# Performance work log

Hardware: AMD Instinct MI355X
Metric: run time of the kernel (lower is better)

Reference implementation:

```python
import jax, jax.numpy as jnp
import numpy as np

N_NODES = 20000
N_EDGES = 400000
DIM = 128       # dim
NB = 16         # radial basis size
ZD = 16         # species encoding dim
N_SPECIES = 51
CUTOFF = 5.0
NLAYERS = 2
N_ONSITE = 3


def radial_basis(r):
    # 'gaussian_rinv': gaussians placed uniformly in inverse-distance space (HIP-NN style)
    rinv = 1.0 / r
    mus = jnp.linspace(1.0 / CUTOFF, 1.0, NB, dtype=r.dtype)
    sigma = mus[1] - mus[0]
    return jnp.exp(-0.5 * ((rinv[:, None] - mus[None, :]) / sigma) ** 2)  # [E, NB]


def setup_inputs() -> dict:
    key = jax.random.key(0)
    ks = jax.random.split(key, 16)
    species = jax.random.randint(ks[0], (N_NODES,), 1, N_SPECIES)
    edge_src = jax.random.randint(ks[1], (N_EDGES,), 0, N_NODES)
    edge_dst = jax.random.randint(ks[2], (N_EDGES,), 0, N_NODES)
    distances = jax.random.uniform(ks[3], (N_EDGES,), minval=0.8, maxval=CUTOFF)
    switch = jax.random.uniform(ks[4], (N_EDGES,))
    Z = jax.random.normal(ks[5], (N_SPECIES, ZD))  # species encoding table
    Ws0 = jax.random.normal(ks[6], (ZD, DIM)) / np.sqrt(ZD)
    bs0 = jnp.zeros((DIM,), jnp.float32)
    V0 = jax.random.normal(ks[7], (NB, ZD, DIM)) / np.sqrt(NB * ZD)
    Ws1 = jax.random.normal(ks[8], (DIM, DIM)) / np.sqrt(DIM)
    bs1 = jnp.zeros((DIM,), jnp.float32)
    V1 = jax.random.normal(ks[9], (NB, DIM, DIM)) / np.sqrt(NB * DIM)
    Won_a = jax.random.normal(ks[10], (NLAYERS, N_ONSITE, DIM, DIM)) / np.sqrt(DIM)
    bon_a = jnp.zeros((NLAYERS, N_ONSITE, DIM), jnp.float32)
    Won_b = jax.random.normal(ks[11], (NLAYERS, N_ONSITE, DIM, DIM)) / np.sqrt(DIM)
    bon_b = jnp.zeros((NLAYERS, N_ONSITE, DIM), jnp.float32)
    return dict(species=species, edge_src=edge_src, edge_dst=edge_dst,
                distances=distances, switch=switch, Z=Z,
                Ws0=Ws0, bs0=bs0, V0=V0, Ws1=Ws1, bs1=bs1, V1=V1,
                Won_a=Won_a, bon_a=bon_a, Won_b=Won_b, bon_b=bon_b)


def reference(species, edge_src, edge_dst, distances, switch, Z,
              Ws0, bs0, V0, Ws1, bs1, V1, Won_a, bon_a, Won_b, bon_b):
    zi = Z[species]                       # [N, ZD] species encoding
    s = radial_basis(distances)           # [E, NB] (identical basis each layer)
    sw = switch[:, None]                  # [E, 1]
    Ws, bs, Vs = (Ws0, Ws1), (bs0, bs1), (V0, V1)
    zis = []
    for layer in range(NLAYERS):
        zself = zi @ Ws[layer] + bs[layer]                        # [N, DIM]
        # mij = einsum('ej,ek,jkl->el', s, zi[edge_dst], V): per-edge outer then one GEMM
        zdst = zi[edge_dst]                                       # [E, k] gather
        outer = s[:, :, None] * zdst[:, None, :]                  # [E, NB, k]
        mij = outer.reshape(outer.shape[0], -1) @ Vs[layer].reshape(-1, DIM)  # [E, DIM]
        zi = jax.nn.silu(zself.at[edge_src].add(mij * sw))        # scatter-add
        for j in range(N_ONSITE):                                 # residual 2-layer MLPs
            h = jax.nn.silu(zi @ Won_a[layer, j] + bon_a[layer, j])
            zi = zi + h @ Won_b[layer, j] + bon_b[layer, j]
        zis.append(zi)
    # (embedding, embedding_layers)
    return zi, jnp.stack(zis, axis=1)
```

## Files before the change

### kernel.cpp

```cpp
#include <hip/hip_runtime.h>
#include <stdint.h>

#define NNODES 20000
#define NEDGES 400000
#define MTILES 1250
#define KS1 68

typedef __attribute__((ext_vector_type(8))) short short8;
typedef __attribute__((ext_vector_type(4))) float floatx4;

__device__ __forceinline__ float bf2f(uint16_t u){ return __uint_as_float(((uint32_t)u)<<16); }
__device__ __forceinline__ uint16_t f2bf(float f){
  uint32_t x = __float_as_uint(f);
  x += 0x7FFFu + ((x>>16)&1u);
  return (uint16_t)(x>>16);
}
__device__ __forceinline__ uint32_t packbf(float a, float b){
  return (uint32_t)f2bf(a) | ((uint32_t)f2bf(b)<<16);
}
__device__ __forceinline__ float siluf(float x){ return x/(1.0f+__expf(-x)); }
__device__ __forceinline__ float ldf(const void* p, int i, int md){
  return (md==1) ? bf2f(((const uint16_t*)p)[i]) : ((const float*)p)[i];
}

#define OFF_V0   0
#define N_V0     32768
#define OFF_WS1  32768
#define N_WS1    16384
#define OFF_BS1  49152
#define N_BS1    128
#define OFF_V1   49280
#define N_V1     262144
#define OFF_WA   311424
#define N_WA     98304
#define OFF_BA   409728
#define N_BA     768
#define OFF_WB   410496
#define N_WB     98304
#define OFF_BB   508800
#define N_BB     768
#define N_CONV   509568

__global__ void k_probe(const void* dist, int* mode){
  if(threadIdx.x != 0 || blockIdx.x != 0) return;
  const float* f = (const float*)dist;
  const uint16_t* h = (const uint16_t*)dist;
  int okf = 1, okb = 1;
  for(int i=0;i<256;i++){
    float a = f[i];       okf &= (a >= 0.7f) & (a <= 5.1f);
    float b = bf2f(h[i]); okb &= (b >= 0.7f) & (b <= 5.1f);
  }
  *mode = okb ? 1 : (okf ? 0 : 1);
}

__global__ __launch_bounds__(256) void k_conv(const void* s0,const void* s1,const void* s2,const void* s3,
                                              const void* s4,const void* s5,const void* s6,const void* s7,
                                              const int* __restrict__ modep, float* __restrict__ dst){
  int md = *modep;
  int i = blockIdx.x*256 + threadIdx.x;
  if(i >= N_CONV) return;
  const void* src; int t = i;
  if(t < N_V0){src=s0;}
  else if((t-=N_V0) < N_WS1){src=s1;}
  else if((t-=N_WS1) < N_BS1){src=s2;}
  else if((t-=N_BS1) < N_V1){src=s3;}
  else if((t-=N_V1) < N_WA){src=s4;}
  else if((t-=N_WA) < N_BA){src=s5;}
  else if((t-=N_BA) < N_WB){src=s6;}
  else {t-=N_WB; src=s7;}
  dst[i] = ldf(src, t, md);
}

__global__ __launch_bounds__(256) void k_hist(const int* __restrict__ src, int* __restrict__ cnt){
  int e = blockIdx.x*256 + threadIdx.x;
  if(e < NEDGES){
    int s = src[e];
    if((unsigned)s < NNODES) atomicAdd(&cnt[s], 1);
  }
}

__global__ __launch_bounds__(1024) void k_scan(int* cnt_cur, int* offs){
  __shared__ int wsum[16];
  int t = threadIdx.x;
  const int chunk = (NNODES + 1023)/1024;
  int lo = t*chunk, hi = lo+chunk;
  if(lo > NNODES) lo = NNODES;
  if(hi > NNODES) hi = NNODES;
  int s = 0;
  for(int i=lo;i<hi;i++) s += cnt_cur[i];
  int lane = t&63, wv = t>>6;
  int v = s;
  #pragma unroll
  for(int d=1; d<64; d<<=1){
    int u = __shfl_up(v, d);
    if(lane >= d) v += u;
  }
  if(lane==63) wsum[wv] = v;
  __syncthreads();
  if(t==0){
    int run = 0;
    #pragma unroll
    for(int i=0;i<16;i++){ int c = wsum[i]; wsum[i] = run; run += c; }
  }
  __syncthreads();
  int run = wsum[wv] + (v - s);
  for(int i=lo;i<hi;i++){
    int c = cnt_cur[i];
    offs[i] = run;
    cnt_cur[i] = run;
    run += c;
  }
  if(t==1023) offs[NNODES] = run;
}

__global__ __launch_bounds__(256) void k_fill(const int* __restrict__ src,
                                              const int* __restrict__ edst,
                                              const int* __restrict__ species,
                                              int* __restrict__ cur,
                                              int* __restrict__ dsts,
                                              int* __restrict__ sps,
                                              int* __restrict__ pos){
  int e = blockIdx.x*256 + threadIdx.x;
  if(e >= NEDGES) return;
  int s = src[e];
  if((unsigned)s >= NNODES) s = 0;
  int p = atomicAdd(&cur[s], 1);
  if((unsigned)p >= NEDGES) p = 0;
  pos[e] = p;
  int dn = edst[e];
  if((unsigned)dn >= NNODES) dn = 0;
  dsts[p] = dn;
  int sp = species[dn];
  if((unsigned)sp >= 51) sp = 0;
  sps[p] = sp;
}

__global__ __launch_bounds__(256) void k_G(const void* __restrict__ dist,
                                           const void* __restrict__ sw,
                                           const int* __restrict__ modep,
                                           const int* __restrict__ pos,
                                           uint16_t* __restrict__ gs){
  int e = blockIdx.x*256 + threadIdx.x;
  if(e >= NEDGES) return;
  int md = *modep;
  float r = ldf(dist, e, md);
  float w = ldf(sw, e, md);
  float rinv = 1.0f/r;
  const float sigma = 0.8f/15.0f;
  const float isig  = 15.0f/0.8f;
  uint32_t u[8];
  #pragma unroll
  for(int j=0;j<8;j++){
    float mu0 = 0.2f + sigma*(float)(2*j);
    float mu1 = 0.2f + sigma*(float)(2*j+1);
    float t0 = (rinv-mu0)*isig, t1 = (rinv-mu1)*isig;
    u[j] = packbf(w*__expf(-0.5f*t0*t0), w*__expf(-0.5f*t1*t1));
  }
  int p = pos[e];
  uint4* o = (uint4*)(gs + (size_t)p*16);
  o[0] = make_uint4(u[0],u[1],u[2],u[3]);
  o[1] = make_uint4(u[4],u[5],u[6],u[7]);
}

__global__ __launch_bounds__(128) void k_spec(const void* __restrict__ Z,
                                              const void* __restrict__ Ws0,
                                              const void* __restrict__ bs0,
                                              const int* __restrict__ modep,
                                              float* __restrict__ ZWs0,
                                              uint16_t* __restrict__ zfb){
  int s = blockIdx.x, d = threadIdx.x;
  int md = *modep;
  float zk[16];
  #pragma unroll
  for(int k=0;k<16;k++) zk[k] = ldf(Z, s*16+k, md);
  float a = ldf(bs0, d, md);
  #pragma unroll
  for(int k=0;k<16;k++) a = fmaf(zk[k], ldf(Ws0, k*128+d, md), a);
  ZWs0[s*128+d] = a;
  if(d < 16) zfb[s*16+d] = f2bf(zk[d]);
}

__global__ __launch_bounds__(256) void k_prepB(const float* __restrict__ W, int Ksteps,
                                               uint16_t* __restrict__ Bf){
  int idx = blockIdx.x*256 + threadIdx.x;
  int total = Ksteps*8*64;
  if(idx >= total) return;
  int l = idx & 63, nt = (idx>>6)&7, kk = idx>>9;
  int kbase = kk*32 + (l>>4)*8;
  int dim = nt*16 + (l&15);
  uint32_t u[4];
  #pragma unroll
  for(int t=0;t<4;t++){
    float f0 = W[(size_t)(kbase+2*t)*128 + dim];
    float f1 = W[(size_t)(kbase+2*t+1)*128 + dim];
    u[t] = packbf(f0,f1);
  }
  ((uint4*)Bf)[idx] = make_uint4(u[0],u[1],u[2],u[3]);
}

__global__ __launch_bounds__(256) void k_prepW(const float* __restrict__ conv,
                                               uint16_t* __restrict__ Wf){
  int idx = blockIdx.x*256 + threadIdx.x;
  if(idx >= 12*2048) return;
  int wi = idx>>11, r = idx&2047;
  int l = r & 63, nt = (r>>6)&7, kk = r>>9;
  const float* W = conv + ((wi<6) ? (OFF_WA + wi*16384) : (OFF_WB + (wi-6)*16384));
  int kbase = kk*32 + (l>>4)*8;
  int dim = nt*16 + (l&15);
  uint32_t u[4];
  #pragma unroll
  for(int t=0;t<4;t++){
    float f0 = W[(size_t)(kbase+2*t)*128 + dim];
    float f1 = W[(size_t)(kbase+2*t+1)*128 + dim];
    u[t] = packbf(f0,f1);
  }
  ((uint4*)Wf)[idx] = make_uint4(u[0],u[1],u[2],u[3]);
}

__global__ __launch_bounds__(256) void k_msg0f(const int* __restrict__ offs,
                                               const int* __restrict__ sps,
                                               const uint16_t* __restrict__ gs,
                                               const uint16_t* __restrict__ zfb,
                                               const uint16_t* __restrict__ Bf,
                                               const int* __restrict__ species,
                                               const float* __restrict__ ZWs0,
                                               float* __restrict__ zi){
  __shared__ uint16_t ldsA[8*64*8];
  int w = threadIdx.x>>6, l = threadIdx.x&63;
  int n0 = blockIdx.x*16;
  int col = l&15, quad = l>>4;
  for(int i=0;i<4;i++){
    int m = w*4 + i;
    int n = n0 + m;
    int beg = offs[n], end = offs[n+1];
    floatx4 acc0 = (floatx4){0.f,0.f,0.f,0.f};
    for(int p0=beg; p0<end; p0+=32){
      int sp[8];
      union { short8 s; uint16_t u[8]; } Bg, Az;
      #pragma unroll
      for(int j=0;j<8;j++){
        int p = p0 + quad*8 + j;
        int pc = p < end ? p : beg;
        sp[j] = sps[pc];
        uint16_t g = gs[(size_t)pc*16 + col];
        Bg.u[j] = (p < end) ? g : (uint16_t)0;
      }
      #pragma unroll
      for(int j=0;j<8;j++)
        Az.u[j] = zfb[sp[j]*16 + col];
      acc0 = __builtin_amdgcn_mfma_f32_16x16x32_bf16(Az.s, Bg.s, acc0, 0,0,0);
    }
    int K0 = col*16 + quad*4;
    int kk = K0>>5, qt = (K0>>3)&3, jt = K0&7;
    int slot = kk*64 + ((qt*16 + m) ^ (kk>>2));
    uint32_t lo = packbf(acc0[0], acc0[1]);
    uint32_t hi = packbf(acc0[2], acc0[3]);
    *(uint2*)(&ldsA[slot*8 + jt]) = make_uint2(lo, hi);
  }
  __syncthreads();
  floatx4 acc1 = (floatx4){0.f,0.f,0.f,0.f};
  floatx4 acc2 = (floatx4){0.f,0.f,0.f,0.f};
  const short8* Bp = (const short8*)Bf;
  int nt1 = w, nt2 = w+4;
  #pragma unroll
  for(int kk=0;kk<8;kk++){
    short8 a = *(const short8*)(&ldsA[(kk*64 + (l^(kk>>2)))*8]);
    short8 b1 = Bp[(size_t)(kk*8+nt1)*64 + l];
    short8 b2 = Bp[(size_t)(kk*8+nt2)*64 + l];
    acc1 = __builtin_amdgcn_mfma_f32_16x16x32_bf16(a, b1, acc1, 0,0,0);
    acc2 = __builtin_amdgcn_mfma_f32_16x16x32_bf16(a, b2, acc2, 0,0,0);
  }
  #pragma unroll
  for(int reg=0;reg<4;reg++){
    int node = n0 + quad*4 + reg;
    int sp = species[node];
    if((unsigned)sp >= 51) sp = 0;
    int d1 = nt1*16 + col, d2 = nt2*16 + col;
    zi[(size_t)node*128 + d1] = siluf(acc1[reg] + ZWs0[sp*128 + d1]);
    zi[(size_t)node*128 + d2] = siluf(acc2[reg] + ZWs0[sp*128 + d2]);
  }
}

__global__ __launch_bounds__(512) void k_msg1f(const int* __restrict__ offs,
                                               const int* __restrict__ dsts,
                                               const uint16_t* __restrict__ gs,
                                               const uint16_t* __restrict__ zib,
                                               const uint16_t* __restrict__ zib2,
                                               const uint16_t* __restrict__ Bf,
                                               const float* __restrict__ bias,
                                               float* __restrict__ zacc){
  __shared__ uint16_t ldsA[64*64*8];
  int w = threadIdx.x>>6, l = threadIdx.x&63;
  int n0 = blockIdx.x*16;
  int col = l&15, quad = l>>4;
  for(int i=0;i<2;i++){
    int m = w*2 + i;
    int n = n0 + m;
    int beg = offs[n], end = offs[n+1];
    floatx4 acc[8];
    #pragma unroll
    for(int t=0;t<8;t++) acc[t] = (floatx4){0.f,0.f,0.f,0.f};
    for(int p0=beg; p0<end; p0+=32){
      int dn[8];
      union { short8 s; uint16_t u[8]; } Bg;
      #pragma unroll
      for(int j=0;j<8;j++){
        int p = p0 + quad*8 + j;
        int pc = p < end ? p : beg;
        dn[j] = dsts[pc];
        uint16_t g = gs[(size_t)pc*16 + col];
        Bg.u[j] = (p < end) ? g : (uint16_t)0;
      }
      uint4 row[8];
      #pragma unroll
      for(int j=0;j<8;j++)
        row[j] = *(const uint4*)(zib2 + (size_t)dn[j]*128 + col*8);
      #pragma unroll
      for(int mt=0;mt<8;mt++){
        union { short8 s; uint32_t u32[4]; } Az;
        #pragma unroll
        for(int cp=0;cp<4;cp++){
          uint32_t a = ((const uint32_t*)&row[2*cp])[mt>>1];
          uint32_t b = ((const uint32_t*)&row[2*cp+1])[mt>>1];
          Az.u32[cp] = __builtin_amdgcn_perm(b, a, (mt&1) ? 0x07060302u : 0x05040100u);
        }
        acc[mt] = __builtin_amdgcn_mfma_f32_16x16x32_bf16(Az.s, Bg.s, acc[mt], 0,0,0);
      }
    }
    #pragma unroll
    for(int mt=0;mt<8;mt++){
      int K0 = col*128 + mt*16 + quad*4;
      int kk = K0>>5, qt = (K0>>3)&3, jt = K0&7;
      int slot = kk*64 + ((qt*16 + m) ^ (kk>>2));
      uint32_t lo = packbf(acc[mt][0], acc[mt][1]);
      uint32_t hi = packbf(acc[mt][2], acc[mt][3]);
      *(uint2*)(&ldsA[slot*8 + jt]) = make_uint2(lo, hi);
    }
  }
  __syncthreads();
  floatx4 acc1 = (floatx4){0.f,0.f,0.f,0.f};
  const short8* Bp = (const short8*)Bf;
  for(int kk=0;kk<64;kk++){
    short8 a = *(const short8*)(&ldsA[(kk*64 + (l^(kk>>2)))*8]);
    short8 b1 = Bp[(size_t)(kk*8+w)*64 + l];
    acc1 = __builtin_amdgcn_mfma_f32_16x16x32_bf16(a, b1, acc1, 0,0,0);
  }
  #pragma unroll
  for(int kk=64;kk<KS1;kk++){
    uint4 za = *(const uint4*)(zib + (size_t)(n0+col)*128 + (kk-64)*32 + quad*8);
    union { short8 s; uint4 u; } A; A.u = za;
    short8 b1 = Bp[(size_t)(kk*8+w)*64 + l];
    acc1 = __builtin_amdgcn_mfma_f32_16x16x32_bf16(A.s, b1, acc1, 0,0,0);
  }
  #pragma unroll
  for(int reg=0;reg<4;reg++){
    int node = n0 + quad*4 + reg;
    int d1 = w*16 + col;
    zacc[(size_t)node*128 + d1] = siluf(acc1[reg] + bias[d1]);
  }
}

__global__ __launch_bounds__(256) void k_onsite(float* __restrict__ zi,
                                                const uint16_t* __restrict__ Waf,
                                                const float* __restrict__ ba,
                                                const uint16_t* __restrict__ Wbf,
                                                const float* __restrict__ bb,
                                                void* __restrict__ outb,
                                                long off1, int st1,
                                                long off2, int st2,
                                                const int* __restrict__ modep,
                                                uint16_t* __restrict__ zib,
                                                uint16_t* __restrict__ zib2){
  __shared__ float zb[16*132];
  __shared__ float hb[16*132];
  int w = threadIdx.x>>6, l = threadIdx.x&63;
  int mtile = blockIdx.x;
  int n0 = mtile*16;
  int md = *modep;
  #pragma unroll
  for(int i=0;i<2;i++){
    int flat = (i*256 + threadIdx.x)*4;
    int node = flat>>7, k = flat&127;
    *(float4*)(zb + node*132 + k) = *(const float4*)(zi + (size_t)(n0+node)*128 + k);
  }
  __syncthreads();
  int m = l&15, q = l>>4;
  for(int j=0;j<3;j++){
    const short8* Ba = (const short8*)Waf + (size_t)j*2048 + l;
    floatx4 acc[2];
    acc[0] = (floatx4){0.f,0.f,0.f,0.f};
    acc[1] = (floatx4){0.f,0.f,0.f,0.f};
    #pragma unroll
    for(int kk=0;kk<4;kk++){
      const float* zp = zb + m*132 + kk*32 + q*8;
      float4 a0 = *(const float4*)zp, a1 = *(const float4*)(zp+4);
      union { short8 s; uint32_t u[4]; } A;
      A.u[0]=packbf(a0.x,a0.y); A.u[1]=packbf(a0.z,a0.w);
      A.u[2]=packbf(a1.x,a1.y); A.u[3]=packbf(a1.z,a1.w);
      #pragma unroll
      for(int t=0;t<2;t++){
        short8 bfr = Ba[(size_t)(kk*8 + w*2+t)*64];
        acc[t] = __builtin_amdgcn_mfma_f32_16x16x32_bf16(A.s, bfr, acc[t], 0,0,0);
      }
    }
    #pragma unroll
    for(int t=0;t<2;t++){
      int dim = (w*2+t)*16 + m;
      float bv = ba[j*128+dim];
      #pragma unroll
      for(int reg=0;reg<4;reg++)
        hb[(q*4+reg)*132 + dim] = siluf(acc[t][reg] + bv);
    }
    __syncthreads();
    const short8* Bb = (const short8*)Wbf + (size_t)j*2048 + l;
    floatx4 acc2[2];
    acc2[0] = (floatx4){0.f,0.f,0.f,0.f};
    acc2[1] = (floatx4){0.f,0.f,0.f,0.f};
    #pragma unroll
    for(int kk=0;kk<4;kk++){
      const float* hp = hb + m*132 + kk*32 + q*8;
      float4 a0 = *(const float4*)hp, a1 = *(const float4*)(hp+4);
      union { short8 s; uint32_t u[4]; } A;
      A.u[0]=packbf(a0.x,a0.y); A.u[1]=packbf(a0.z,a0.w);
      A.u[2]=packbf(a1.x,a1.y); A.u[3]=packbf(a1.z,a1.w);
      #pragma unroll
      for(int t=0;t<2;t++){
        short8 bfr = Bb[(size_t)(kk*8 + w*2+t)*64];
        acc2[t] = __builtin_amdgcn_mfma_f32_16x16x32_bf16(A.s, bfr, acc2[t], 0,0,0);
      }
    }
    #pragma unroll
    for(int t=0;t<2;t++){
      int dim = (w*2+t)*16 + m;
      float bv = bb[j*128+dim];
      #pragma unroll
      for(int reg=0;reg<4;reg++){
        int idx = (q*4+reg)*132 + dim;
        zb[idx] = zb[idx] + acc2[t][reg] + bv;
      }
    }
    __syncthreads();
  }
  #pragma unroll
  for(int i=0;i<2;i++){
    int flat = (i*256 + threadIdx.x)*4;
    int node = flat>>7, k = flat&127;
    float4 v = *(float4*)(zb + node*132 + k);
    int n = n0 + node;
    *(float4*)(zi + (size_t)n*128 + k) = v;
    uint2 pv = make_uint2(packbf(v.x,v.y), packbf(v.z,v.w));
    if(zib) *(uint2*)(zib + (size_t)n*128 + k) = pv;
    if(md==1){
      uint16_t* ob = (uint16_t*)outb;
      *(uint2*)(ob + off1 + (long)n*st1 + k) = pv;
      if(off2 >= 0) *(uint2*)(ob + off2 + (long)n*st2 + k) = pv;
    } else {
      float* ob = (float*)outb;
      *(float4*)(ob + off1 + (long)n*st1 + k) = v;
      if(off2 >= 0) *(float4*)(ob + off2 + (long)n*st2 + k) = v;
    }
  }
  if(zib2){
    int node2 = threadIdx.x>>4, c = threadIdx.x&15;
    float vv[8];
    #pragma unroll
    for(int mt=0;mt<8;mt++) vv[mt] = zb[node2*132 + mt*16 + c];
    uint4 o = make_uint4(packbf(vv[0],vv[1]), packbf(vv[2],vv[3]),
                         packbf(vv[4],vv[5]), packbf(vv[6],vv[7]));
    *(uint4*)(zib2 + (size_t)(n0+node2)*128 + c*8) = o;
  }
}

extern "C" void kernel_launch(void* const* d_in, const int* in_sizes, int n_in,
                              void* d_out, int out_size, void* d_ws, size_t ws_size,
                              hipStream_t stream){
  const int* species = (const int*)d_in[0];
  const int* esrc    = (const int*)d_in[1];
  const int* edst    = (const int*)d_in[2];
  const void* dist   = d_in[3];
  const void* swit   = d_in[4];
  const void* Z      = d_in[5];
  const void* Ws0    = d_in[6];
  const void* bs0    = d_in[7];
  const void* V0     = d_in[8];
  const void* Ws1    = d_in[9];
  const void* bs1    = d_in[10];
  const void* V1     = d_in[11];
  const void* Wa     = d_in[12];
  const void* ba     = d_in[13];
  const void* Wb     = d_in[14];
  const void* bb     = d_in[15];

  char* ws = (char*)d_ws;
  size_t off = 0;
  auto alloc = [&](size_t bytes)->void*{ void* p = ws + off; off = (off + bytes + 255) & ~(size_t)255; return p; };
  int*      offs = (int*)     alloc((size_t)(NNODES+1)*4);
  int*      cur  = (int*)     alloc((size_t)NNODES*4);
  int*      pos  = (int*)     alloc((size_t)NEDGES*4);
  int*      dsts = (int*)     alloc((size_t)NEDGES*4);
  int*      sps  = (int*)     alloc((size_t)NEDGES*4);
  uint16_t* gs   = (uint16_t*)alloc((size_t)NEDGES*16*2);
  float*    zi   = (float*)   alloc((size_t)NNODES*128*4);
  float*    zacc = (float*)   alloc((size_t)NNODES*128*4);
  uint16_t* zib  = (uint16_t*)alloc((size_t)NNODES*128*2);
  uint16_t* zib2 = (uint16_t*)alloc((size_t)NNODES*128*2);
  float*    ZWs0 = (float*)   alloc((size_t)51*128*4);
  uint16_t* zfb  = (uint16_t*)alloc((size_t)51*16*2);
  float*    conv = (float*)   alloc((size_t)N_CONV*4);
  uint16_t* Bf0  = (uint16_t*)alloc((size_t)8*8*64*8*2);
  uint16_t* Bf1  = (uint16_t*)alloc((size_t)KS1*8*64*8*2);
  uint16_t* Wfr  = (uint16_t*)alloc((size_t)12*16384*2);
  int*      mode = (int*)     alloc(256);

  const int EB = (NEDGES+255)/256;
  hipMemsetAsync(cur, 0, NNODES*4, stream);
  k_probe<<<1,64,0,stream>>>(dist, mode);
  k_conv <<<(N_CONV+255)/256,256,0,stream>>>(V0, Ws1, bs1, V1, Wa, ba, Wb, bb, mode, conv);
  k_hist <<<EB,256,0,stream>>>(esrc, cur);
  k_scan <<<1,1024,0,stream>>>(cur, offs);
  k_fill <<<EB,256,0,stream>>>(esrc, edst, species, cur, dsts, sps, pos);
  k_G    <<<EB,256,0,stream>>>(dist, swit, mode, pos, gs);
  k_spec <<<51,128,0,stream>>>(Z, Ws0, bs0, mode, ZWs0, zfb);
  k_prepB<<<(8*8*64+255)/256,256,0,stream>>>(conv+OFF_V0, 8,  Bf0);
  k_prepB<<<(64*8*64+255)/256,256,0,stream>>>(conv+OFF_V1, 64, Bf1);
  k_prepB<<<(4*8*64+255)/256,256,0,stream>>>(conv+OFF_WS1, 4, Bf1 + (size_t)64*8*64*8);
  k_prepW<<<(12*2048+255)/256,256,0,stream>>>(conv, Wfr);

  const long ZIS = (long)NNODES*128;
  uint16_t* WaF0 = Wfr;
  uint16_t* WaF1 = Wfr + (size_t)3*16384;
  uint16_t* WbF0 = Wfr + (size_t)6*16384;
  uint16_t* WbF1 = Wfr + (size_t)9*16384;

  k_msg0f<<<MTILES,256,0,stream>>>(offs, sps, gs, zfb, Bf0, species, ZWs0, zi);
  k_onsite<<<MTILES,256,0,stream>>>(zi, WaF0, conv+OFF_BA, WbF0, conv+OFF_BB,
                                    d_out, ZIS, 256, (long)-1, 0, mode, zib, zib2);

  k_msg1f<<<MTILES,512,0,stream>>>(offs, dsts, gs, zib, zib2, Bf1, conv+OFF_BS1, zacc);
  k_onsite<<<MTILES,256,0,stream>>>(zacc, WaF1, conv+OFF_BA+384, WbF1, conv+OFF_BB+384,
                                    d_out, ZIS+128, 256, (long)0, 128, mode,
                                    (uint16_t*)nullptr, (uint16_t*)nullptr);
}
```

Baseline: 304.4 us.

## Double k_msg1f block to 1024 threads with one node per wave and split-K GEMM

```diff
diff --git a/kernel.cpp b/kernel.cpp
--- a/kernel.cpp
+++ b/kernel.cpp
@@ -281,7 +281,7 @@
   }
 }
 
-__global__ __launch_bounds__(512) void k_msg1f(const int* __restrict__ offs,
+__global__ __launch_bounds__(1024, 8) void k_msg1f(const int* __restrict__ offs,
                                                const int* __restrict__ dsts,
                                                const uint16_t* __restrict__ gs,
                                                const uint16_t* __restrict__ zib,
@@ -289,12 +289,12 @@
                                                const uint16_t* __restrict__ Bf,
                                                const float* __restrict__ bias,
                                                float* __restrict__ zacc){
-  __shared__ uint16_t ldsA[64*64*8];
+  __shared__ __align__(16) uint16_t ldsA[64*64*8];
   int w = threadIdx.x>>6, l = threadIdx.x&63;
   int n0 = blockIdx.x*16;
   int col = l&15, quad = l>>4;
-  for(int i=0;i<2;i++){
-    int m = w*2 + i;
+  {
+    int m = w;
     int n = n0 + m;
     int beg = offs[n], end = offs[n+1];
     floatx4 acc[8];
@@ -338,25 +338,38 @@
     }
   }
   __syncthreads();
+  int nt1 = w & 7, half = w >> 3;
   floatx4 acc1 = (floatx4){0.f,0.f,0.f,0.f};
   const short8* Bp = (const short8*)Bf;
-  for(int kk=0;kk<64;kk++){
+  int kb = half*32, ke = kb + 32;
+  #pragma unroll 8
+  for(int kk=kb;kk<ke;kk++){
     short8 a = *(const short8*)(&ldsA[(kk*64 + (l^(kk>>2)))*8]);
-    short8 b1 = Bp[(size_t)(kk*8+w)*64 + l];
+    short8 b1 = Bp[(size_t)(kk*8+nt1)*64 + l];
     acc1 = __builtin_amdgcn_mfma_f32_16x16x32_bf16(a, b1, acc1, 0,0,0);
   }
   #pragma unroll
-  for(int kk=64;kk<KS1;kk++){
+  for(int t=0;t<2;t++){
+    int kk = 64 + half*2 + t;
     uint4 za = *(const uint4*)(zib + (size_t)(n0+col)*128 + (kk-64)*32 + quad*8);
     union { short8 s; uint4 u; } A; A.u = za;
-    short8 b1 = Bp[(size_t)(kk*8+w)*64 + l];
+    short8 b1 = Bp[(size_t)(kk*8+nt1)*64 + l];
     acc1 = __builtin_amdgcn_mfma_f32_16x16x32_bf16(A.s, b1, acc1, 0,0,0);
   }
-  #pragma unroll
-  for(int reg=0;reg<4;reg++){
-    int node = n0 + quad*4 + reg;
-    int d1 = w*16 + col;
-    zacc[(size_t)node*128 + d1] = siluf(acc1[reg] + bias[d1]);
+  __syncthreads();
+  float* red = (float*)ldsA;
+  if(half==1){
+    *(floatx4*)(&red[(nt1*64 + l)*4]) = acc1;
+  }
+  __syncthreads();
+  if(half==0){
+    floatx4 o = *(const floatx4*)(&red[(nt1*64 + l)*4]);
+    #pragma unroll
+    for(int reg=0;reg<4;reg++){
+      int node = n0 + quad*4 + reg;
+      int d1 = nt1*16 + col;
+      zacc[(size_t)node*128 + d1] = siluf(acc1[reg] + o[reg] + bias[d1]);
+    }
   }
 }
 
@@ -536,7 +549,7 @@
   k_onsite<<<MTILES,256,0,stream>>>(zi, WaF0, conv+OFF_BA, WbF0, conv+OFF_BB,
                                     d_out, ZIS, 256, (long)-1, 0, mode, zib, zib2);
 
-  k_msg1f<<<MTILES,512,0,stream>>>(offs, dsts, gs, zib, zib2, Bf1, conv+OFF_BS1, zacc);
+  k_msg1f<<<MTILES,1024,0,stream>>>(offs, dsts, gs, zib, zib2, Bf1, conv+OFF_BS1, zacc);
   k_onsite<<<MTILES,256,0,stream>>>(zacc, WaF1, conv+OFF_BA+384, WbF1, conv+OFF_BB+384,
                                     d_out, ZIS+128, 256, (long)0, 128, mode,
                                     (uint16_t*)nullptr, (uint16_t*)nullptr);
```

Result: slower. 340.2 us (+11.7%).
